# Performance work log

Measured on AMD Instinct MI355X. Metric: run time of the kernel, lower is better.

The kernel has to match this reference:

```python
import jax, jax.numpy as jnp
import numpy as np

L, D, DB, P, B = 33, 2048, 1024, 24, 2048
EPS = 1e-5

def _ln(x, g, b):
    # LayerNorm over last axis, eps matches torch default 1e-5
    mu = jnp.mean(x, axis=-1, keepdims=True)
    var = jnp.mean(jnp.square(x - mu), axis=-1, keepdims=True)
    return (x - mu) * jax.lax.rsqrt(var + EPS) * g + b

def setup_inputs() -> dict:
    key = jax.random.key(0)
    ks = jax.random.split(key, 8)
    s1 = 1.0 / np.sqrt(D)   # fan-in style scaling to keep activations sane
    s2 = 1.0 / np.sqrt(DB)
    sp = 1.0 / np.sqrt(P)
    return {
        "x":      jax.random.normal(ks[0], (B, L, D), jnp.float32),
        "pos_emb": jax.random.uniform(ks[1], (L, P), jnp.float32),
        "Wk":     jax.random.normal(ks[2], (P, D), jnp.float32) * sp,
        "W1":     jax.random.normal(ks[3], (L, D, DB), jnp.float32) * s1,
        "b1":     jnp.zeros((L, DB), jnp.float32),
        "ln1_g":  jnp.ones((L, DB), jnp.float32),
        "ln1_b":  jnp.zeros((L, DB), jnp.float32),
        "W2":     jax.random.normal(ks[4], (L, DB, D), jnp.float32) * s2,
        "b2":     jnp.zeros((L, D), jnp.float32),
        "ln2_g":  jnp.ones((L, D), jnp.float32),
        "ln2_b":  jnp.zeros((L, D), jnp.float32),
        "Wq1":    jax.random.normal(ks[5], (D, DB), jnp.float32) * s1,
        "bq1":    jnp.zeros((DB,), jnp.float32),
        "lnq_g":  jnp.ones((DB,), jnp.float32),
        "lnq_b":  jnp.zeros((DB,), jnp.float32),
        "Wq2":    jax.random.normal(ks[6], (DB, D), jnp.float32) * s2,
        "bq2":    jnp.zeros((D,), jnp.float32),
    }

def reference(x, pos_emb, Wk, W1, b1, ln1_g, ln1_b, W2, b2, ln2_g, ln2_b,
              Wq1, bq1, lnq_g, lnq_b, Wq2, bq2):
    # x: [B, L, D]
    z_L = x[:, -1, :]                                   # [B, D]
    keys = pos_emb @ Wk                                 # Eq.10: [L, D]
    # Eq.11 + Eq.4: per-layer value MLPs, grouped as batched GEMMs
    h = jax.nn.gelu(jnp.einsum('bld,ldk->blk', x, W1) + b1, approximate=False)
    h = _ln(h, ln1_g, ln1_b)                            # [B, L, DB]
    v = jnp.einsum('blk,lkd->bld', h, W2) + b2          # [B, L, D]
    values = _ln(v, ln2_g, ln2_b)                       # [B, L, D]
    # Eq.5: query from last layer
    hq = jax.nn.gelu(z_L @ Wq1 + bq1, approximate=False)
    hq = _ln(hq, lnq_g, lnq_b)
    q_tr = hq @ Wq2 + bq2                               # [B, D]
    query = 1.0 + jax.nn.elu(z_L + q_tr)                # [B, D]
    # Eq.7-9: single-query attention over depth + residual
    attn = jax.nn.softmax(query @ keys.T, axis=-1)      # [B, L]
    attended = jnp.einsum('bl,bld->bd', attn, values)   # [B, D]
    return z_L + attended
```

## Files before the change

### kernel.cpp

```cpp
#include <hip/hip_runtime.h>
#include <cstddef>
#include <cstdint>

#define Lc 33
#define Dc 2048
#define DBc 1024
#define Pc 24
#define Bc 2048

typedef __attribute__((ext_vector_type(4))) float f32x4;
typedef __attribute__((ext_vector_type(8))) short s16x8;
typedef __attribute__((ext_vector_type(4))) short s16x4;

__device__ __forceinline__ short bf16r(float f) {
  unsigned u = __float_as_uint(f);
  u = (u + 0x7fffu + ((u >> 16) & 1u)) >> 16;
  return (short)u;
}
__device__ __forceinline__ float bf2f(short s) {
  return __uint_as_float(((unsigned)(unsigned short)s) << 16);
}
__device__ __forceinline__ s16x8 pack8(const float* f) {
  s16x8 r;
#pragma unroll
  for (int i = 0; i < 8; ++i) r[i] = bf16r(f[i]);
  return r;
}
__device__ __forceinline__ void split8(const float* f, s16x8& hi, s16x8& lo) {
#pragma unroll
  for (int i = 0; i < 8; ++i) {
    short h = bf16r(f[i]);
    hi[i] = h;
    lo[i] = bf16r(f[i] - bf2f(h));
  }
}
__device__ __forceinline__ void gl_lds16(const void* g, void* l) {
  __builtin_amdgcn_global_load_lds(
      (const __attribute__((address_space(1))) unsigned int*)g,
      (__attribute__((address_space(3))) unsigned int*)l, 16, 0, 0);
}

__global__ __launch_bounds__(256)
void keys_kernel(const float* __restrict__ pe, const float* __restrict__ Wk,
                 float* __restrict__ keys) {
  const int l = blockIdx.x;
  const int d = blockIdx.y * 256 + threadIdx.x;
  float s = 0.f;
#pragma unroll
  for (int p = 0; p < Pc; ++p) s += pe[l * Pc + p] * Wk[(size_t)p * Dc + d];
  keys[(size_t)l * Dc + d] = s;
}

template <int K, int N>
__global__ __launch_bounds__(256)
void transpose_w(const float* __restrict__ W, unsigned short* __restrict__ Wt) {
  const int z = blockIdx.z;
  const int k0 = blockIdx.x * 64, n0 = blockIdx.y * 64;
  __shared__ unsigned short tile[64][66];
  const int t = threadIdx.x;
  {
    const int r = t >> 2, cq = (t & 3) * 16;
    const float* src = W + (size_t)z * K * N + (size_t)(k0 + r) * N + n0 + cq;
#pragma unroll
    for (int i = 0; i < 16; i += 4) {
      f32x4 v = *(const f32x4*)(src + i);
#pragma unroll
      for (int j = 0; j < 4; ++j)
        tile[r][cq + i + j] = (unsigned short)bf16r(v[j]);
    }
  }
  __syncthreads();
  {
    const int n = t >> 2, kc = (t & 3) * 16;
    s16x8 o0, o1;
#pragma unroll
    for (int i = 0; i < 8; ++i) {
      o0[i] = tile[kc + i][n];
      o1[i] = tile[kc + 8 + i][n];
    }
    unsigned short* dst =
        Wt + (size_t)z * N * K + (size_t)(n0 + n) * K + k0 + kc;
    *(s16x8*)dst = o0;
    *(s16x8*)(dst + 8) = o1;
  }
}

template <int MODE>
__global__ __launch_bounds__(256, 2)
void gemm_bf16(const float* __restrict__ xsrc,
               const unsigned short* __restrict__ hsrc,
               const unsigned short* __restrict__ Wt,
               const float* __restrict__ bias,
               unsigned short* __restrict__ outbuf) {
  constexpr int K = (MODE == 1) ? 2048 : 1024;
  constexpr int N = (MODE == 1) ? 1024 : 2048;
  constexpr int NT = K / 64;
  const int z = blockIdx.z, bm = blockIdx.x, bn = blockIdx.y;
  const int tid = threadIdx.x, lane = tid & 63, w = tid >> 6;
  const int wr = (w >> 1) * 64, wc = (w & 1) * 64;
  const int l15 = lane & 15, kb = lane >> 4;

  __shared__ __align__(16) unsigned short Als[128 * 64];
  __shared__ __align__(16) unsigned short Bls[128 * 64];

  f32x4 acc[4][4];
#pragma unroll
  for (int m = 0; m < 4; ++m)
#pragma unroll
    for (int n = 0; n < 4; ++n) {
      acc[m][n][0] = 0.f; acc[m][n][1] = 0.f;
      acc[m][n][2] = 0.f; acc[m][n][3] = 0.f;
    }

  const int rl8 = lane >> 3;
  const int sl = lane & 7;
  const int swzE = ((sl ^ rl8) << 3);

  const unsigned short* Bbase = Wt + (size_t)z * N * K;

  const int ar = tid >> 1, ahalf = tid & 1;
  const float* ApF = nullptr;
  if constexpr (MODE == 1) {
    ApF = xsrc + (size_t)(bm * 128 + ar) * (Lc * Dc) + (size_t)z * Dc +
          ahalf * 32;
  }

  for (int kt = 0; kt < NT; ++kt) {
    f32x4 av[8];
    if constexpr (MODE == 1) {
      const float* p = ApF + kt * 64;
#pragma unroll
      for (int i = 0; i < 8; ++i) av[i] = *(const f32x4*)(p + i * 4);
    } else {
#pragma unroll
      for (int j = 0; j < 4; ++j) {
        const int rloc = w * 32 + j * 8 + rl8;
        const unsigned short* g =
            hsrc + ((size_t)(bm * 128 + rloc) * Lc + z) * DBc + kt * 64 + swzE;
        gl_lds16(g, (char*)Als + w * 4096 + j * 1024);
      }
    }
#pragma unroll
    for (int j = 0; j < 4; ++j) {
      const int rloc = w * 32 + j * 8 + rl8;
      const unsigned short* g =
          Bbase + (size_t)(bn * 128 + rloc) * K + kt * 64 + swzE;
      gl_lds16(g, (char*)Bls + w * 4096 + j * 1024);
    }
    if constexpr (MODE == 1) {
#pragma unroll
      for (int c = 0; c < 4; ++c) {
        float f[8];
#pragma unroll
        for (int j = 0; j < 4; ++j) {
          f[j] = av[2 * c][j];
          f[4 + j] = av[2 * c + 1][j];
        }
        s16x8 pk = pack8(f);
        const int s = ahalf * 4 + c;
        *(s16x8*)((char*)Als + ar * 128 + ((s ^ (ar & 7)) << 4)) = pk;
      }
    }
    __syncthreads();
#pragma unroll
    for (int kk = 0; kk < 2; ++kk) {
      s16x8 af[4], bfv[4];
#pragma unroll
      for (int m = 0; m < 4; ++m) {
        const int row = wr + m * 16 + l15;
        const int slot = kk * 4 + kb;
        af[m] = *(const s16x8*)((const char*)Als + row * 128 +
                                ((slot ^ (row & 7)) << 4));
      }
#pragma unroll
      for (int n = 0; n < 4; ++n) {
        const int row = wc + n * 16 + l15;
        const int slot = kk * 4 + kb;
        bfv[n] = *(const s16x8*)((const char*)Bls + row * 128 +
                                 ((slot ^ (row & 7)) << 4));
      }
#pragma unroll
      for (int m = 0; m < 4; ++m)
#pragma unroll
        for (int n = 0; n < 4; ++n)
          acc[m][n] = __builtin_amdgcn_mfma_f32_16x16x32_bf16(
              af[m], bfv[n], acc[m][n], 0, 0, 0);
    }
    __syncthreads();
  }

  const float* biasP = bias + (size_t)z * N;
#pragma unroll
  for (int m = 0; m < 4; ++m) {
    const int r0 = bm * 128 + wr + m * 16 + kb * 4;
#pragma unroll
    for (int n = 0; n < 4; ++n) {
      const int col = bn * 128 + wc + n * 16 + l15;
      const float bs = biasP[col];
#pragma unroll
      for (int j = 0; j < 4; ++j) {
        const int r = r0 + j;
        const float v = acc[m][n][j] + bs;
        if constexpr (MODE == 1) {
          const float g = 0.5f * v * (1.0f + erff(v * 0.70710678118f));
          outbuf[((size_t)r * Lc + z) * DBc + col] = (unsigned short)bf16r(g);
        } else {
          outbuf[((size_t)r * Lc + z) * Dc + col] = (unsigned short)bf16r(v);
        }
      }
    }
  }
}

template <int MODE, int SPLITQ>
__global__ __launch_bounds__(256, 2)
void gemm_fused(const float* __restrict__ x,
                const unsigned short* __restrict__ hbuf,
                const float* __restrict__ hqF,
                const float* __restrict__ Wmain, const float* __restrict__ Wq,
                const float* __restrict__ bmain, const float* __restrict__ bq,
                unsigned short* __restrict__ outH, float* __restrict__ outHq,
                unsigned short* __restrict__ outV, float* __restrict__ outQ) {
  constexpr int K = (MODE == 1) ? 2048 : 1024;
  constexpr int N = (MODE == 1) ? 1024 : 2048;
  constexpr int BK = 32;
  constexpr int NT = K / BK;

  const int z = blockIdx.z;
  const int bm = blockIdx.x;
  const int bn = blockIdx.y;
  const int tid = threadIdx.x;
  const int lane = tid & 63;
  const int wid = tid >> 6;
  const int wr = (wid >> 1) * 64;
  const int wc = (wid & 1) * 64;
  const int l15 = lane & 15;
  const int kb = lane >> 4;

  const float* Bp = SPLITQ ? Wq : (Wmain + (size_t)z * K * N);

  __shared__ short Als[1 + SPLITQ][128][32];
  __shared__ short Bls[1 + SPLITQ][128][32];

  const f32x4 vzero = {0.f, 0.f, 0.f, 0.f};
  f32x4 acc[4][4];
#pragma unroll
  for (int m = 0; m < 4; ++m)
#pragma unroll
    for (int n = 0; n < 4; ++n) acc[m][n] = vzero;

  const int ar = tid >> 1;
  const int ak = (tid & 1) * 16;
  const int grow = bm * 128 + ar;

  const float* ApF = nullptr;
  const unsigned short* ApH = nullptr;
  if constexpr (MODE == 1) {
    const int lsel = SPLITQ ? (Lc - 1) : z;
    ApF = x + (size_t)grow * (Lc * Dc) + (size_t)lsel * Dc + ak;
  } else if constexpr (SPLITQ == 1) {
    ApF = hqF + (size_t)grow * DBc + ak;
  } else {
    ApH = hbuf + ((size_t)grow * 33 + z) * DBc + ak;
  }

  const int bnL = tid & 127;
  const int bj = tid >> 7;
  const int c0 = ((bnL >> 1) & 3) ^ bj;
  const int kc0 = c0 * 8;
  const int kc1 = (c0 ^ 2) * 8;
  const float* Bcol = Bp + (size_t)bn * 128 + bnL;

  float aF[16];
  s16x8 aH0, aH1;
  float bF[16];

  auto loadA = [&](int kt) {
    if constexpr (MODE == 2 && SPLITQ == 0) {
      const unsigned short* p = ApH + kt * BK;
      aH0 = *(const s16x8*)p;
      aH1 = *(const s16x8*)(p + 8);
    } else {
      const float* p = ApF + kt * BK;
#pragma unroll
      for (int i = 0; i < 4; ++i) {
        f32x4 t = *(const f32x4*)(p + i * 4);
#pragma unroll
        for (int j = 0; j < 4; ++j) aF[i * 4 + j] = t[j];
      }
    }
  };
  auto loadB = [&](int kt) {
    const float* p0 = Bcol + (size_t)(kt * BK + kc0) * N;
    const float* p1 = Bcol + (size_t)(kt * BK + kc1) * N;
#pragma unroll
    for (int i = 0; i < 8; ++i) bF[i] = p0[(size_t)i * N];
#pragma unroll
    for (int i = 0; i < 8; ++i) bF[8 + i] = p1[(size_t)i * N];
  };
  auto writeLDS = [&]() {
    if constexpr (MODE == 2 && SPLITQ == 0) {
      *(s16x8*)&Als[0][ar][ak] = aH0;
      *(s16x8*)&Als[0][ar][ak + 8] = aH1;
    } else if constexpr (SPLITQ == 0) {
      *(s16x8*)&Als[0][ar][ak] = pack8(aF);
      *(s16x8*)&Als[0][ar][ak + 8] = pack8(aF + 8);
    } else {
      s16x8 h0, l0, h1, l1;
      split8(aF, h0, l0);
      split8(aF + 8, h1, l1);
      *(s16x8*)&Als[0][ar][ak] = h0;
      *(s16x8*)&Als[1][ar][ak] = l0;
      *(s16x8*)&Als[0][ar][ak + 8] = h1;
      *(s16x8*)&Als[1][ar][ak + 8] = l1;
    }
    if constexpr (SPLITQ == 0) {
      *(s16x8*)&Bls[0][bnL][kc0] = pack8(bF);
      *(s16x8*)&Bls[0][bnL][kc1] = pack8(bF + 8);
    } else {
      s16x8 h0, l0, h1, l1;
      split8(bF, h0, l0);
      split8(bF + 8, h1, l1);
      *(s16x8*)&Bls[0][bnL][kc0] = h0;
      *(s16x8*)&Bls[1][bnL][kc0] = l0;
      *(s16x8*)&Bls[0][bnL][kc1] = h1;
      *(s16x8*)&Bls[1][bnL][kc1] = l1;
    }
  };

  loadA(0);
  loadB(0);
  for (int kt = 0; kt < NT; ++kt) {
    __syncthreads();
    writeLDS();
    if (kt + 1 < NT) {
      loadA(kt + 1);
      loadB(kt + 1);
    }
    __syncthreads();
    s16x8 af[4], bfv[4];
#pragma unroll
    for (int m = 0; m < 4; ++m)
      af[m] = *(const s16x8*)&Als[0][wr + m * 16 + l15][kb * 8];
#pragma unroll
    for (int n = 0; n < 4; ++n)
      bfv[n] = *(const s16x8*)&Bls[0][wc + n * 16 + l15][kb * 8];
    if constexpr (SPLITQ == 1) {
      s16x8 afl[4], bfl[4];
#pragma unroll
      for (int m = 0; m < 4; ++m)
        afl[m] = *(const s16x8*)&Als[1][wr + m * 16 + l15][kb * 8];
#pragma unroll
      for (int n = 0; n < 4; ++n)
        bfl[n] = *(const s16x8*)&Bls[1][wc + n * 16 + l15][kb * 8];
#pragma unroll
      for (int m = 0; m < 4; ++m)
#pragma unroll
        for (int n = 0; n < 4; ++n) {
          acc[m][n] = __builtin_amdgcn_mfma_f32_16x16x32_bf16(
              af[m], bfv[n], acc[m][n], 0, 0, 0);
          acc[m][n] = __builtin_amdgcn_mfma_f32_16x16x32_bf16(
              af[m], bfl[n], acc[m][n], 0, 0, 0);
          acc[m][n] = __builtin_amdgcn_mfma_f32_16x16x32_bf16(
              afl[m], bfv[n], acc[m][n], 0, 0, 0);
        }
    } else {
#pragma unroll
      for (int m = 0; m < 4; ++m)
#pragma unroll
        for (int n = 0; n < 4; ++n)
          acc[m][n] = __builtin_amdgcn_mfma_f32_16x16x32_bf16(
              af[m], bfv[n], acc[m][n], 0, 0, 0);
    }
  }

  const float* biasP = SPLITQ ? bq : (bmain + (size_t)z * N);
#pragma unroll
  for (int m = 0; m < 4; ++m) {
    const int r0 = bm * 128 + wr + m * 16 + kb * 4;
#pragma unroll
    for (int n = 0; n < 4; ++n) {
      const int col = bn * 128 + wc + n * 16 + l15;
      const float bs = biasP[col];
#pragma unroll
      for (int j = 0; j < 4; ++j) {
        const int r = r0 + j;
        const float v = acc[m][n][j] + bs;
        if constexpr (MODE == 1 && SPLITQ == 0) {
          const float g = 0.5f * v * (1.0f + erff(v * 0.70710678118f));
          outH[((size_t)r * 33 + z) * DBc + col] = (unsigned short)bf16r(g);
        } else if constexpr (MODE == 1 && SPLITQ == 1) {
          const float g = 0.5f * v * (1.0f + erff(v * 0.70710678118f));
          outHq[(size_t)r * DBc + col] = g;
        } else if constexpr (MODE == 2 && SPLITQ == 0) {
          outV[((size_t)r * 33 + z) * Dc + col] = (unsigned short)bf16r(v);
        } else {
          const float zl =
              x[(size_t)r * (Lc * Dc) + (size_t)(Lc - 1) * Dc + col];
          const float t = zl + v;
          outQ[(size_t)r * Dc + col] = (t > 0.f) ? (1.f + t) : __expf(t);
        }
      }
    }
  }
}

template <int W>
__global__ __launch_bounds__(256)
void ln_kernel(unsigned short* __restrict__ buf, const float* __restrict__ gmain,
               const float* __restrict__ bmain) {
  constexpr int E = W / 256;
  const int z = blockIdx.x;
  const int b = blockIdx.y;
  const int tid = threadIdx.x;
  unsigned short* row = buf + ((size_t)b * 33 + z) * W;
  float v[E];
  if constexpr (E == 4) {
    s16x4 t = *(const s16x4*)(row + tid * 4);
#pragma unroll
    for (int i = 0; i < 4; ++i) v[i] = bf2f(t[i]);
  } else {
    s16x8 t = *(const s16x8*)(row + tid * 8);
#pragma unroll
    for (int i = 0; i < 8; ++i) v[i] = bf2f(t[i]);
  }
  float s = 0.f, s2 = 0.f;
#pragma unroll
  for (int i = 0; i < E; ++i) {
    s += v[i];
    s2 += v[i] * v[i];
  }
#pragma unroll
  for (int o = 32; o > 0; o >>= 1) {
    s += __shfl_xor(s, o);
    s2 += __shfl_xor(s2, o);
  }
  __shared__ float red[2][4];
  const int w = tid >> 6;
  if ((tid & 63) == 0) {
    red[0][w] = s;
    red[1][w] = s2;
  }
  __syncthreads();
  s = red[0][0] + red[0][1] + red[0][2] + red[0][3];
  s2 = red[1][0] + red[1][1] + red[1][2] + red[1][3];
  const float mu = s * (1.0f / W);
  const float var = s2 * (1.0f / W) - mu * mu;
  const float rstd = rsqrtf(var + 1e-5f);
  const float* G = gmain + (size_t)z * W;
  const float* Bt = bmain + (size_t)z * W;
  if constexpr (E == 4) {
    f32x4 gv = *(const f32x4*)(G + tid * 4);
    f32x4 bv = *(const f32x4*)(Bt + tid * 4);
    s16x4 o;
#pragma unroll
    for (int i = 0; i < 4; ++i)
      o[i] = bf16r((v[i] - mu) * rstd * gv[i] + bv[i]);
    *(s16x4*)(row + tid * 4) = o;
  } else {
    f32x4 g0 = *(const f32x4*)(G + tid * 8);
    f32x4 g1 = *(const f32x4*)(G + tid * 8 + 4);
    f32x4 b0 = *(const f32x4*)(Bt + tid * 8);
    f32x4 b1 = *(const f32x4*)(Bt + tid * 8 + 4);
    s16x8 o;
#pragma unroll
    for (int i = 0; i < 4; ++i) {
      o[i] = bf16r((v[i] - mu) * rstd * g0[i] + b0[i]);
      o[i + 4] = bf16r((v[i + 4] - mu) * rstd * g1[i] + b1[i]);
    }
    *(s16x8*)(row + tid * 8) = o;
  }
}

__global__ __launch_bounds__(256)
void ln_f32_kernel(float* __restrict__ buf, const float* __restrict__ g,
                   const float* __restrict__ bb) {
  const int r = blockIdx.x;
  const int tid = threadIdx.x;
  float* row = buf + (size_t)r * DBc;
  f32x4 v = *(const f32x4*)(row + tid * 4);
  float s = 0.f, s2 = 0.f;
#pragma unroll
  for (int i = 0; i < 4; ++i) {
    s += v[i];
    s2 += v[i] * v[i];
  }
#pragma unroll
  for (int o = 32; o > 0; o >>= 1) {
    s += __shfl_xor(s, o);
    s2 += __shfl_xor(s2, o);
  }
  __shared__ float red[2][4];
  const int w = tid >> 6;
  if ((tid & 63) == 0) {
    red[0][w] = s;
    red[1][w] = s2;
  }
  __syncthreads();
  s = red[0][0] + red[0][1] + red[0][2] + red[0][3];
  s2 = red[1][0] + red[1][1] + red[1][2] + red[1][3];
  const float mu = s * (1.0f / DBc);
  const float var = s2 * (1.0f / DBc) - mu * mu;
  const float rstd = rsqrtf(var + 1e-5f);
  f32x4 gv = *(const f32x4*)(g + tid * 4);
  f32x4 bv = *(const f32x4*)(bb + tid * 4);
  f32x4 o;
#pragma unroll
  for (int i = 0; i < 4; ++i) o[i] = (v[i] - mu) * rstd * gv[i] + bv[i];
  *(f32x4*)(row + tid * 4) = o;
}

__global__ __launch_bounds__(256)
void attn_kernel(const float* __restrict__ x, const float* __restrict__ query,
                 const float* __restrict__ keys,
                 const unsigned short* __restrict__ vals,
                 float* __restrict__ out) {
  const int b = blockIdx.x;
  const int tid = threadIdx.x;
  const int d0 = tid * 8;

  float q[8];
  {
    f32x4 t0 = *(const f32x4*)(query + (size_t)b * Dc + d0);
    f32x4 t1 = *(const f32x4*)(query + (size_t)b * Dc + d0 + 4);
#pragma unroll
    for (int i = 0; i < 4; ++i) {
      q[i] = t0[i];
      q[i + 4] = t1[i];
    }
  }
  float s[33];
#pragma unroll
  for (int l = 0; l < 33; ++l) {
    const float* kp = keys + (size_t)l * Dc + d0;
    f32x4 k0 = *(const f32x4*)kp;
    f32x4 k1 = *(const f32x4*)(kp + 4);
    float t = 0.f;
#pragma unroll
    for (int i = 0; i < 4; ++i) t += q[i] * k0[i] + q[i + 4] * k1[i];
    s[l] = t;
  }
#pragma unroll
  for (int l = 0; l < 33; ++l) {
    float v = s[l];
#pragma unroll
    for (int o = 32; o > 0; o >>= 1) v += __shfl_xor(v, o);
    s[l] = v;
  }
  __shared__ float sred[4][33];
  __shared__ float sl[33];
  const int w = tid >> 6;
  if ((tid & 63) == 0) {
#pragma unroll
    for (int l = 0; l < 33; ++l) sred[w][l] = s[l];
  }
  __syncthreads();
  if (tid < 33)
    sl[tid] = sred[0][tid] + sred[1][tid] + sred[2][tid] + sred[3][tid];
  __syncthreads();

  float m = -1e30f;
#pragma unroll
  for (int l = 0; l < 33; ++l) m = fmaxf(m, sl[l]);
  float p[33];
  float sum = 0.f;
#pragma unroll
  for (int l = 0; l < 33; ++l) {
    p[l] = __expf(sl[l] - m);
    sum += p[l];
  }
  const float inv = 1.0f / sum;

  float acc8[8];
  {
    const float* zl = x + (size_t)b * (Lc * Dc) + (size_t)(Lc - 1) * Dc + d0;
    f32x4 z0 = *(const f32x4*)zl;
    f32x4 z1 = *(const f32x4*)(zl + 4);
#pragma unroll
    for (int i = 0; i < 4; ++i) {
      acc8[i] = z0[i];
      acc8[i + 4] = z1[i];
    }
  }
  const unsigned short* vb = vals + (size_t)b * 33 * Dc + d0;
#pragma unroll
  for (int l = 0; l < 33; ++l) {
    s16x8 vv = *(const s16x8*)(vb + (size_t)l * Dc);
    const float a = p[l] * inv;
#pragma unroll
    for (int i = 0; i < 8; ++i) acc8[i] += a * bf2f(vv[i]);
  }
  f32x4 o0, o1;
#pragma unroll
  for (int i = 0; i < 4; ++i) {
    o0[i] = acc8[i];
    o1[i] = acc8[i + 4];
  }
  *(f32x4*)(out + (size_t)b * Dc + d0) = o0;
  *(f32x4*)(out + (size_t)b * Dc + d0 + 4) = o1;
}

extern "C" void kernel_launch(void* const* d_in, const int* in_sizes, int n_in,
                              void* d_out, int out_size, void* d_ws,
                              size_t ws_size, hipStream_t stream) {
  const float* x = (const float*)d_in[0];
  const float* pe = (const float*)d_in[1];
  const float* Wk = (const float*)d_in[2];
  const float* W1 = (const float*)d_in[3];
  const float* b1 = (const float*)d_in[4];
  const float* ln1g = (const float*)d_in[5];
  const float* ln1b = (const float*)d_in[6];
  const float* W2 = (const float*)d_in[7];
  const float* b2 = (const float*)d_in[8];
  const float* ln2g = (const float*)d_in[9];
  const float* ln2b = (const float*)d_in[10];
  const float* Wq1 = (const float*)d_in[11];
  const float* bq1 = (const float*)d_in[12];
  const float* lnqg = (const float*)d_in[13];
  const float* lnqb = (const float*)d_in[14];
  const float* Wq2 = (const float*)d_in[15];
  const float* bq2 = (const float*)d_in[16];
  float* out = (float*)d_out;
  char* ws = (char*)d_ws;

  float* keysP = (float*)(ws);
  float* queryP = (float*)(ws + 270336);
  float* hqP = (float*)(ws + 17047552);
  unsigned short* hP = (unsigned short*)(ws + 25436160);
  unsigned short* valsP = (unsigned short*)(ws + 163848192);
  unsigned short* W1tP = (unsigned short*)(ws + 163848192);
  unsigned short* W2tP = (unsigned short*)(ws + 440672256);

  const bool fast = (ws_size >= 579084288ull);

  keys_kernel<<<dim3(33, 8), 256, 0, stream>>>(pe, Wk, keysP);

  gemm_fused<1, 1><<<dim3(16, 8, 1), 256, 0, stream>>>(
      x, nullptr, nullptr, nullptr, Wq1, nullptr, bq1, nullptr, hqP, nullptr,
      nullptr);

  if (fast) {
    transpose_w<2048, 1024><<<dim3(32, 16, 33), 256, 0, stream>>>(W1, W1tP);
    gemm_bf16<1><<<dim3(16, 8, 33), 256, 0, stream>>>(x, nullptr, W1tP, b1,
                                                      hP);
  } else {
    gemm_fused<1, 0><<<dim3(16, 8, 33), 256, 0, stream>>>(
        x, nullptr, nullptr, W1, nullptr, b1, nullptr, hP, nullptr, nullptr,
        nullptr);
  }

  ln_kernel<1024><<<dim3(33, 2048), 256, 0, stream>>>(hP, ln1g, ln1b);

  ln_f32_kernel<<<dim3(2048), 256, 0, stream>>>(hqP, lnqg, lnqb);

  if (fast) {
    transpose_w<1024, 2048><<<dim3(16, 32, 33), 256, 0, stream>>>(W2, W2tP);
    gemm_bf16<2><<<dim3(16, 16, 33), 256, 0, stream>>>(nullptr, hP, W2tP, b2,
                                                       valsP);
  } else {
    gemm_fused<2, 0><<<dim3(16, 16, 33), 256, 0, stream>>>(
        x, hP, nullptr, W2, nullptr, b2, nullptr, nullptr, nullptr, valsP,
        nullptr);
  }

  gemm_fused<2, 1><<<dim3(16, 16, 1), 256, 0, stream>>>(
      x, nullptr, hqP, nullptr, Wq2, nullptr, bq2, nullptr, nullptr, nullptr,
      queryP);

  ln_kernel<2048><<<dim3(33, 2048), 256, 0, stream>>>(valsP, ln2g, ln2b);

  attn_kernel<<<dim3(2048), 256, 0, stream>>>(x, queryP, keysP, valsP, out);
}
```

Before: 1.763 ms.

## Pre-convert x to bf16 and double-buffer LDS in batched bf16 GEMMs

Adds a separate kernel that converts the whole fp32 input x to bf16 into workspace. Both batched GEMMs can then load A and B directly to LDS with global_load_lds. The GEMM now double-buffers its LDS tiles so the next k-tile loads while MFMAs run on the current one, with one barrier per iteration instead of two. The cost is an extra pass over x (about 0.5 GB read plus a bf16 write) and twice the LDS per block, which may lower occupancy. W1t is moved to a different workspace region so it does not overlap the bf16 copy of x.

Result: faster. 1.722 ms (-2.3%).

```diff
diff --git a/kernel.cpp b/kernel.cpp
--- a/kernel.cpp
+++ b/kernel.cpp
@@ -38,6 +38,16 @@
   __builtin_amdgcn_global_load_lds(
       (const __attribute__((address_space(1))) unsigned int*)g,
       (__attribute__((address_space(3))) unsigned int*)l, 16, 0, 0);
+}
+
+__global__ __launch_bounds__(256)
+void cvt_bf16_kernel(const float* __restrict__ in,
+                     unsigned short* __restrict__ outp) {
+  const size_t i = ((size_t)blockIdx.x * 256 + threadIdx.x) * 8;
+  f32x4 a = *(const f32x4*)(in + i);
+  f32x4 b = *(const f32x4*)(in + i + 4);
+  float f[8] = {a[0], a[1], a[2], a[3], b[0], b[1], b[2], b[3]};
+  *(s16x8*)(outp + i) = pack8(f);
 }
 
 __global__ __launch_bounds__(256)
@@ -85,23 +95,20 @@
   }
 }
 
-template <int MODE>
+template <int K, int N, int GELU>
 __global__ __launch_bounds__(256, 2)
-void gemm_bf16(const float* __restrict__ xsrc,
-               const unsigned short* __restrict__ hsrc,
-               const unsigned short* __restrict__ Wt,
-               const float* __restrict__ bias,
-               unsigned short* __restrict__ outbuf) {
-  constexpr int K = (MODE == 1) ? 2048 : 1024;
-  constexpr int N = (MODE == 1) ? 1024 : 2048;
+void gemm2ph(const unsigned short* __restrict__ A,
+             const unsigned short* __restrict__ Wt,
+             const float* __restrict__ bias,
+             unsigned short* __restrict__ outbuf) {
   constexpr int NT = K / 64;
   const int z = blockIdx.z, bm = blockIdx.x, bn = blockIdx.y;
   const int tid = threadIdx.x, lane = tid & 63, w = tid >> 6;
   const int wr = (w >> 1) * 64, wc = (w & 1) * 64;
   const int l15 = lane & 15, kb = lane >> 4;
 
-  __shared__ __align__(16) unsigned short Als[128 * 64];
-  __shared__ __align__(16) unsigned short Bls[128 * 64];
+  __shared__ __align__(16) unsigned short Als[2][128 * 64];
+  __shared__ __align__(16) unsigned short Bls[2][128 * 64];
 
   f32x4 acc[4][4];
 #pragma unroll
@@ -112,56 +119,29 @@
       acc[m][n][2] = 0.f; acc[m][n][3] = 0.f;
     }
 
-  const int rl8 = lane >> 3;
-  const int sl = lane & 7;
+  const int rl8 = lane >> 3, sl = lane & 7;
   const int swzE = ((sl ^ rl8) << 3);
 
   const unsigned short* Bbase = Wt + (size_t)z * N * K;
 
-  const int ar = tid >> 1, ahalf = tid & 1;
-  const float* ApF = nullptr;
-  if constexpr (MODE == 1) {
-    ApF = xsrc + (size_t)(bm * 128 + ar) * (Lc * Dc) + (size_t)z * Dc +
-          ahalf * 32;
-  }
-
-  for (int kt = 0; kt < NT; ++kt) {
-    f32x4 av[8];
-    if constexpr (MODE == 1) {
-      const float* p = ApF + kt * 64;
-#pragma unroll
-      for (int i = 0; i < 8; ++i) av[i] = *(const f32x4*)(p + i * 4);
-    } else {
-#pragma unroll
-      for (int j = 0; j < 4; ++j) {
-        const int rloc = w * 32 + j * 8 + rl8;
-        const unsigned short* g =
-            hsrc + ((size_t)(bm * 128 + rloc) * Lc + z) * DBc + kt * 64 + swzE;
-        gl_lds16(g, (char*)Als + w * 4096 + j * 1024);
-      }
-    }
+  auto stage = [&](int buf, int kt) {
 #pragma unroll
     for (int j = 0; j < 4; ++j) {
       const int rloc = w * 32 + j * 8 + rl8;
-      const unsigned short* g =
-          Bbase + (size_t)(bn * 128 + rloc) * K + kt * 64 + swzE;
-      gl_lds16(g, (char*)Bls + w * 4096 + j * 1024);
-    }
-    if constexpr (MODE == 1) {
-#pragma unroll
-      for (int c = 0; c < 4; ++c) {
-        float f[8];
-#pragma unroll
-        for (int j = 0; j < 4; ++j) {
-          f[j] = av[2 * c][j];
-          f[4 + j] = av[2 * c + 1][j];
-        }
-        s16x8 pk = pack8(f);
-        const int s = ahalf * 4 + c;
-        *(s16x8*)((char*)Als + ar * 128 + ((s ^ (ar & 7)) << 4)) = pk;
-      }
-    }
-    __syncthreads();
+      gl_lds16(A + ((size_t)(bm * 128 + rloc) * Lc + z) * K + kt * 64 + swzE,
+               (char*)&Als[buf][0] + w * 4096 + j * 1024);
+      gl_lds16(Bbase + (size_t)(bn * 128 + rloc) * K + kt * 64 + swzE,
+               (char*)&Bls[buf][0] + w * 4096 + j * 1024);
+    }
+  };
+
+  stage(0, 0);
+  asm volatile("s_waitcnt vmcnt(0)" ::: "memory");
+  __builtin_amdgcn_s_barrier();
+
+  for (int kt = 0; kt < NT; ++kt) {
+    const int cur = kt & 1;
+    if (kt + 1 < NT) stage(cur ^ 1, kt + 1);
 #pragma unroll
     for (int kk = 0; kk < 2; ++kk) {
       s16x8 af[4], bfv[4];
@@ -169,14 +149,14 @@
       for (int m = 0; m < 4; ++m) {
         const int row = wr + m * 16 + l15;
         const int slot = kk * 4 + kb;
-        af[m] = *(const s16x8*)((const char*)Als + row * 128 +
+        af[m] = *(const s16x8*)((const char*)&Als[cur][0] + row * 128 +
                                 ((slot ^ (row & 7)) << 4));
       }
 #pragma unroll
       for (int n = 0; n < 4; ++n) {
         const int row = wc + n * 16 + l15;
         const int slot = kk * 4 + kb;
-        bfv[n] = *(const s16x8*)((const char*)Bls + row * 128 +
+        bfv[n] = *(const s16x8*)((const char*)&Bls[cur][0] + row * 128 +
                                  ((slot ^ (row & 7)) << 4));
       }
 #pragma unroll
@@ -186,7 +166,8 @@
           acc[m][n] = __builtin_amdgcn_mfma_f32_16x16x32_bf16(
               af[m], bfv[n], acc[m][n], 0, 0, 0);
     }
-    __syncthreads();
+    asm volatile("s_waitcnt vmcnt(0)" ::: "memory");
+    __builtin_amdgcn_s_barrier();
   }
 
   const float* biasP = bias + (size_t)z * N;
@@ -200,13 +181,9 @@
 #pragma unroll
       for (int j = 0; j < 4; ++j) {
         const int r = r0 + j;
-        const float v = acc[m][n][j] + bs;
-        if constexpr (MODE == 1) {
-          const float g = 0.5f * v * (1.0f + erff(v * 0.70710678118f));
-          outbuf[((size_t)r * Lc + z) * DBc + col] = (unsigned short)bf16r(g);
-        } else {
-          outbuf[((size_t)r * Lc + z) * Dc + col] = (unsigned short)bf16r(v);
-        }
+        float v = acc[m][n][j] + bs;
+        if constexpr (GELU) v = 0.5f * v * (1.0f + erff(v * 0.70710678118f));
+        outbuf[((size_t)r * Lc + z) * N + col] = (unsigned short)bf16r(v);
       }
     }
   }
@@ -627,8 +604,9 @@
   float* queryP = (float*)(ws + 270336);
   float* hqP = (float*)(ws + 17047552);
   unsigned short* hP = (unsigned short*)(ws + 25436160);
+  unsigned short* xbfP = (unsigned short*)(ws + 163848192);
   unsigned short* valsP = (unsigned short*)(ws + 163848192);
-  unsigned short* W1tP = (unsigned short*)(ws + 163848192);
+  unsigned short* W1tP = (unsigned short*)(ws + 440672256);
   unsigned short* W2tP = (unsigned short*)(ws + 440672256);
 
   const bool fast = (ws_size >= 579084288ull);
@@ -640,9 +618,10 @@
       nullptr);
 
   if (fast) {
+    cvt_bf16_kernel<<<dim3(67584), 256, 0, stream>>>(x, xbfP);
     transpose_w<2048, 1024><<<dim3(32, 16, 33), 256, 0, stream>>>(W1, W1tP);
-    gemm_bf16<1><<<dim3(16, 8, 33), 256, 0, stream>>>(x, nullptr, W1tP, b1,
-                                                      hP);
+    gemm2ph<2048, 1024, 1><<<dim3(16, 8, 33), 256, 0, stream>>>(xbfP, W1tP,
+                                                                b1, hP);
   } else {
     gemm_fused<1, 0><<<dim3(16, 8, 33), 256, 0, stream>>>(
         x, nullptr, nullptr, W1, nullptr, b1, nullptr, hP, nullptr, nullptr,
@@ -655,8 +634,8 @@
 
   if (fast) {
     transpose_w<1024, 2048><<<dim3(16, 32, 33), 256, 0, stream>>>(W2, W2tP);
-    gemm_bf16<2><<<dim3(16, 16, 33), 256, 0, stream>>>(nullptr, hP, W2tP, b2,
-                                                       valsP);
+    gemm2ph<1024, 2048, 0><<<dim3(16, 16, 33), 256, 0, stream>>>(hP, W2tP, b2,
+                                                                 valsP);
   } else {
     gemm_fused<2, 0><<<dim3(16, 16, 33), 256, 0, stream>>>(
         x, hP, nullptr, W2, nullptr, b2, nullptr, nullptr, nullptr, valsP,
```
